# Kernel tuning notes

Measured on AMD Instinct MI355X. Metric: run time of the kernel, lower is better.

The kernel has to match this reference:

```python
import jax, jax.numpy as jnp
import numpy as np

QMIN, QMAX = 0.0, 255.0
# activation statistics (min, max) per layer, from init_kwargs['stats']
STATS = {"conv1": (-0.5, 3.0), "conv2": (0.0, 6.0), "fc1": (0.0, 8.0), "fc2": (0.0, 10.0)}


def calc_scale_zp(min_val, max_val):
    scale = (max_val - min_val) / (QMAX - QMIN)
    # original: int(clamped initial zero point) -> truncation
    zp = jnp.trunc(jnp.clip(QMIN - min_val / scale, QMIN, QMAX))
    return scale, zp


def quantize(x, min_val=None, max_val=None):
    if min_val is None:
        min_val, max_val = x.min(), x.max()
    scale, zp = calc_scale_zp(min_val, max_val)
    q = jnp.round(jnp.clip(zp + x / scale, QMIN, QMAX))
    return q, scale, zp


def conv2d(x, w, b):
    y = jax.lax.conv_general_dilated(x, w, (1, 1), "VALID",
                                     dimension_numbers=("NCHW", "OIHW", "NCHW"))
    return y + b[None, :, None, None]


def linear(x, w, b):
    return x @ w.T + b


def max_pool_2x2(x):
    return jax.lax.reduce_window(x, -jnp.inf, jax.lax.max, (1, 1, 2, 2), (1, 1, 2, 2), "VALID")


def quantize_layer(q_x, scale_x, zp_x, W, B, apply_fn, stat):
    # fake-quant weights/bias with their own min/max
    wq, scale_w, zp_w = quantize(W)
    bq, scale_b, zp_b = quantize(B)
    scale_next, zp_next = calc_scale_zp(stat[0], stat[1])
    X = q_x - zp_x
    W_eff = scale_x * scale_w * (wq - zp_w)
    B_eff = scale_b * (bq + zp_b)  # '+ zp_b' is faithful to the source
    y = jax.nn.relu(apply_fn(X, W_eff, B_eff) / scale_next + zp_next)
    # .round().byte() in torch wraps mod 256
    return jnp.mod(jnp.round(y), 256.0), scale_next, zp_next


def setup_inputs() -> dict:
    key = jax.random.key(0)
    ks = jax.random.split(key, 9)
    B = 4096
    return {
        "x": jax.random.normal(ks[0], (B, 1, 28, 28), jnp.float32),
        "conv1_w": jax.random.normal(ks[1], (20, 1, 5, 5), jnp.float32) * 0.1,
        "conv1_b": jax.random.normal(ks[2], (20,), jnp.float32) * 0.1,
        "conv2_w": jax.random.normal(ks[3], (50, 20, 5, 5), jnp.float32) * 0.05,
        "conv2_b": jax.random.normal(ks[4], (50,), jnp.float32) * 0.05,
        "fc1_w": jax.random.normal(ks[5], (500, 800), jnp.float32) * 0.03,
        "fc1_b": jax.random.normal(ks[6], (500,), jnp.float32) * 0.03,
        "fc2_w": jax.random.normal(ks[7], (10, 500), jnp.float32) * 0.05,
        "fc2_b": jax.random.normal(ks[8], (10,), jnp.float32) * 0.05,
    }


def reference(x, conv1_w, conv1_b, conv2_w, conv2_b, fc1_w, fc1_b, fc2_w, fc2_b):
    q, s, zp = quantize(x, STATS["conv1"][0], STATS["conv1"][1])
    q, s, zp = quantize_layer(q, s, zp, conv1_w, conv1_b, conv2d, STATS["conv2"])
    q = max_pool_2x2(q)                       # [B,20,12,12]
    q, s, zp = quantize_layer(q, s, zp, conv2_w, conv2_b, conv2d, STATS["fc1"])
    q = max_pool_2x2(q)                       # [B,50,4,4]
    q = q.reshape(-1, 4 * 4 * 50)             # [B,800]
    q, s, zp = quantize_layer(q, s, zp, fc1_w, fc1_b, linear, STATS["fc2"])
    xf = s * (q - zp)                         # dequantize
    logits = linear(xf, fc2_w, fc2_b)         # [B,10]
    return jax.nn.log_softmax(logits, axis=1)
```

## Files before the change

kernel.cpp:

```cpp
#include <hip/hip_runtime.h>
#include <cmath>

#define TPB 256
typedef float floatx4 __attribute__((ext_vector_type(4)));
typedef __bf16 bf16x8 __attribute__((ext_vector_type(8)));
typedef unsigned short ushort8 __attribute__((ext_vector_type(8)));
typedef unsigned short ushort_t;

#define OFF_PMN 16
#define OFF_PMX 96
#define OFF_B1 520
#define OFF_B2 544
#define OFF_B3 600
#define W1BF_BYTE 6144
#define W2BF_BYTE 8192
#define W3BF_BYTE 131072
#define Q2_BYTE  29360128ULL

#define S_X1 (3.5f/255.0f)
#define ZP_X1 36.0f
#define S_N1 (6.0f/255.0f)
#define S_N2 (8.0f/255.0f)
#define S_N3 (10.0f/255.0f)

#define XSTR 40

__device__ inline float qclip(float x, float s, float zp){
    return rintf(fminf(fmaxf(zp + x / s, 0.0f), 255.0f));
}
__device__ inline ushort_t bfbits(float v){
    return (ushort_t)(__float_as_uint(v) >> 16);
}

__global__ __launch_bounds__(TPB) void k_minmax(
        const float* c1w, const float* c1b, const float* c2w, const float* c2b,
        const float* f1w, const float* f1b, float* pmn, float* pmx){
    __shared__ float smn[TPB], smx[TPB];
    int bb = blockIdx.x, tid = threadIdx.x;
    const float* src; int n, sub, nsub;
    if      (bb == 0){ src=c1w; n=500;    sub=0;     nsub=1;  }
    else if (bb == 1){ src=c1b; n=20;     sub=0;     nsub=1;  }
    else if (bb <  6){ src=c2w; n=25000;  sub=bb-2;  nsub=4;  }
    else if (bb == 6){ src=c2b; n=50;     sub=0;     nsub=1;  }
    else if (bb < 71){ src=f1w; n=400000; sub=bb-7;  nsub=64; }
    else             { src=f1b; n=500;    sub=0;     nsub=1;  }
    float mn = INFINITY, mx = -INFINITY;
    for (int i = sub*TPB + tid; i < n; i += nsub*TPB){
        float v = src[i]; mn = fminf(mn, v); mx = fmaxf(mx, v);
    }
    smn[tid] = mn; smx[tid] = mx; __syncthreads();
    for (int s = TPB/2; s > 0; s >>= 1){
        if (tid < s){
            smn[tid] = fminf(smn[tid], smn[tid+s]);
            smx[tid] = fmaxf(smx[tid], smx[tid+s]);
        }
        __syncthreads();
    }
    if (tid == 0){ pmn[bb] = smn[0]; pmx[bb] = smx[0]; }
}

#define N_EFF 452157
__global__ __launch_bounds__(TPB) void k_make_eff(
        const float* c1w, const float* c1b, const float* c2w, const float* c2b,
        const float* f1w, const float* f1b, const float* pmn, const float* pmx,
        float* ws, ushort_t* w1bf, ushort_t* w2bf, ushort_t* w3bf){
    __shared__ float sS[6], sZ[6];
    int tid = threadIdx.x;
    int wv = tid >> 6, lane = tid & 63;
    const int starts[6] = {0,1,2,6,7,71};
    const int counts[6] = {1,1,4,1,64,1};
    #pragma unroll
    for (int rep = 0; rep < 2; ++rep){
        int t = wv + rep*4;
        if (t < 6){
            float mn = INFINITY, mx = -INFINITY;
            if (lane < counts[t]){ mn = pmn[starts[t]+lane]; mx = pmx[starts[t]+lane]; }
            #pragma unroll
            for (int off = 32; off > 0; off >>= 1){
                mn = fminf(mn, __shfl_xor(mn, off));
                mx = fmaxf(mx, __shfl_xor(mx, off));
            }
            if (lane == 0){
                float s = (mx - mn) / 255.0f;
                sS[t] = s;
                sZ[t] = truncf(fminf(fmaxf(0.0f - mn / s, 0.0f), 255.0f));
            }
        }
    }
    __syncthreads();

    int i = blockIdx.x * TPB + tid;
    if (i >= N_EFF) return;
    if (i < 1024){
        int n = i >> 5, k = i & 31;
        float v = 0.0f;
        if (n < 20 && k < 25) v = qclip(c1w[n*25 + k], sS[0], sZ[0]) - sZ[0];
        w1bf[i] = bfbits(v);
    } else if (i < 1044){
        int j = i - 1024;
        ws[OFF_B1 + j] = (sS[1] * (qclip(c1b[j], sS[1], sZ[1]) + sZ[1])) / S_N1;
    } else if (i < 42004){
        int j = i - 1044;
        int c = j >> 11, r = j & 2047, co = r >> 5, k = r & 31;
        int q = k >> 3, jj = k & 7;
        int tap, ci; bool valid;
        if (c < 13){ tap = 2*c + (q>>1); ci = (q&1)*8 + jj; valid = (tap < 25); }
        else       { tap = 4*(c-13) + q; ci = 16 + jj;      valid = (tap < 25) && (jj < 4); }
        valid = valid && (co < 50);
        float v = 0.0f;
        if (valid) v = qclip(c2w[(co*20 + ci)*25 + tap], sS[2], sZ[2]) - sZ[2];
        w2bf[j] = bfbits(v);
    } else if (i < 42054){
        int j = i - 42004;
        ws[OFF_B2 + j] = (sS[3] * (qclip(c2b[j], sS[3], sZ[3]) + sZ[3])) / S_N2;
    } else if (i < 451654){
        int j = i - 42054;
        int n = j / 800, k = j - 800*n;
        float v = 0.0f;
        if (n < 500) v = qclip(f1w[n*800 + k], sS[4], sZ[4]) - sZ[4];
        w3bf[j] = bfbits(v);
    } else if (i < 452154){
        int j = i - 451654;
        ws[OFF_B3 + j] = (sS[5] * (qclip(f1b[j], sS[5], sZ[5]) + sZ[5])) / S_N3;
    } else if (i == 452154){
        ws[0] = (S_N1 * sS[2]) / S_N2;
    } else if (i == 452155){
        ws[1] = (S_N2 * sS[4]) / S_N3;
    } else {
        ws[2] = (S_X1 * sS[0]) / S_N1;
    }
}

__global__ __launch_bounds__(TPB) void k_conv12(const float* x, const ushort_t* w1bf,
                                                const ushort_t* w2bt, const float* ws,
                                                ushort_t* q2bf, int B){
    __shared__ __align__(16) ushort_t xs[144*XSTR];
    __shared__ __align__(16) ushort_t xim[3136];
    int b = blockIdx.x, tid = threadIdx.x;
    int lane = tid & 63, wv = tid >> 6;
    int ln = lane & 15, quad = lane >> 4;

    for (int i = tid; i < 144; i += TPB){
        *(unsigned int*)(xs + i*XSTR + 20) = 0u;
        *(unsigned int*)(xs + i*XSTR + 22) = 0u;
    }

    const float* xb = x + (size_t)b * 784;
    for (int i = tid; i < 784; i += TPB){
        float v = xb[i];
        float q = rintf(fminf(fmaxf(ZP_X1 + v / S_X1, 0.0f), 255.0f));
        ushort_t bits = bfbits(q - ZP_X1);
        xim[i] = bits; xim[784 + i] = bits; xim[1568 + i] = bits; xim[2352 + i] = bits;
    }

    int offj[8]; bool vj[8];
    #pragma unroll
    for (int j = 0; j < 8; ++j){
        int k = quad*8 + j;
        vj[j] = (k < 25);
        int kh = k / 5, kw = k - 5*kh;
        offj[j] = vj[j] ? (kh*28 + kw) : 0;
    }
    const ushort_t* xq = xim + quad*784;

    ushort8 bw0 = *(const ushort8*)(w1bf + ln*32 + quad*8);
    ushort8 bw1 = *(const ushort8*)(w1bf + (16 + ln)*32 + quad*8);
    bf16x8 bf0 = __builtin_bit_cast(bf16x8, bw0);
    bf16x8 bf1 = __builtin_bit_cast(bf16x8, bw1);

    float K1 = ws[2];
    float B1_0 = ws[OFF_B1 + ln];
    float B1_1 = (ln < 4) ? ws[OFF_B1 + 16 + ln] : 0.0f;
    __syncthreads();

    for (int i = 0; i < 9; ++i){
        int mt = 9*wv + i;
        int m = mt*16 + ln;
        int p = m >> 2, crn = m & 3;
        int ph_ = p / 12, pw_ = p - 12*ph_;
        int oh = 2*ph_ + (crn >> 1), ow = 2*pw_ + (crn & 1);
        int base = oh*28 + ow;
        ushort8 aw;
        #pragma unroll
        for (int j = 0; j < 8; ++j)
            aw[j] = vj[j] ? xq[base + offj[j]] : (ushort_t)0;
        bf16x8 af = __builtin_bit_cast(bf16x8, aw);
        floatx4 z = (floatx4){0.f,0.f,0.f,0.f};
        floatx4 a0 = __builtin_amdgcn_mfma_f32_16x16x32_bf16(af, bf0, z, 0, 0, 0);
        floatx4 a1 = __builtin_amdgcn_mfma_f32_16x16x32_bf16(af, bf1, z, 0, 0, 0);

        int pp = mt*4 + quad;
        {
            unsigned int qv[4];
            #pragma unroll
            for (int r = 0; r < 4; ++r){
                float y = fmaxf(fmaf(a0[r], K1, B1_0), 0.0f);
                qv[r] = ((unsigned int)rintf(y)) & 255u;
            }
            unsigned int h0 = qv[0] > qv[1] ? qv[0] : qv[1];
            unsigned int h1 = qv[2] > qv[3] ? qv[2] : qv[3];
            unsigned int mx = h0 > h1 ? h0 : h1;
            xs[pp*XSTR + ln] = bfbits((float)mx);
        }
        if (ln < 4){
            unsigned int qv[4];
            #pragma unroll
            for (int r = 0; r < 4; ++r){
                float y = fmaxf(fmaf(a1[r], K1, B1_1), 0.0f);
                qv[r] = ((unsigned int)rintf(y)) & 255u;
            }
            unsigned int h0 = qv[0] > qv[1] ? qv[0] : qv[1];
            unsigned int h1 = qv[2] > qv[3] ? qv[2] : qv[3];
            unsigned int mx = h0 > h1 ? h0 : h1;
            xs[pp*XSTR + 16 + ln] = bfbits((float)mx);
        }
    }
    __syncthreads();

    int mt0 = (wv & 1) * 2;
    int nt0 = (wv >> 1) * 2;
    int abase[2];
    #pragma unroll
    for (int mi = 0; mi < 2; ++mi)
        abase[mi] = (24*(mt0+mi) + (ln>>3)*12 + (ln&7)) * XSTR;
    int aoff[20];
    #pragma unroll
    for (int c = 0; c < 20; ++c){
        int tap, inner;
        if (c < 13){ tap = 2*c + (quad>>1); inner = (quad&1)*8; }
        else       { tap = 4*(c-13) + quad; inner = 16; }
        int pt = 0;
        if (tap < 25){ int kh = tap/5, kw = tap-5*kh; pt = kh*12 + kw; }
        aoff[c] = pt*XSTR + inner;
    }

    float sc2d = ws[0];
    const ushort_t* bsrc0 = w2bt + (size_t)(nt0*16 + ln)*32 + quad*8;
    const ushort_t* bsrc1 = bsrc0 + 16*32;

    floatx4 acc[2][2];
    #pragma unroll
    for (int mi = 0; mi < 2; ++mi)
        #pragma unroll
        for (int ni = 0; ni < 2; ++ni) acc[mi][ni] = (floatx4){0.f,0.f,0.f,0.f};

    #pragma unroll
    for (int c = 0; c < 20; ++c){
        ushort8 b0w = *(const ushort8*)(bsrc0 + c*2048);
        ushort8 b1w = *(const ushort8*)(bsrc1 + c*2048);
        ushort8 a0w = *(const ushort8*)(xs + abase[0] + aoff[c]);
        ushort8 a1w = *(const ushort8*)(xs + abase[1] + aoff[c]);
        bf16x8 a0 = __builtin_bit_cast(bf16x8, a0w);
        bf16x8 a1 = __builtin_bit_cast(bf16x8, a1w);
        bf16x8 b0 = __builtin_bit_cast(bf16x8, b0w);
        bf16x8 b1 = __builtin_bit_cast(bf16x8, b1w);
        acc[0][0] = __builtin_amdgcn_mfma_f32_16x16x32_bf16(a0, b0, acc[0][0], 0, 0, 0);
        acc[0][1] = __builtin_amdgcn_mfma_f32_16x16x32_bf16(a0, b1, acc[0][1], 0, 0, 0);
        acc[1][0] = __builtin_amdgcn_mfma_f32_16x16x32_bf16(a1, b0, acc[1][0], 0, 0, 0);
        acc[1][1] = __builtin_amdgcn_mfma_f32_16x16x32_bf16(a1, b1, acc[1][1], 0, 0, 0);
    }

    #pragma unroll
    for (int ni = 0; ni < 2; ++ni){
        int co = (nt0 + ni)*16 + ln;
        float bias2d = (co < 50) ? ws[OFF_B2 + co] : 0.0f;
        #pragma unroll
        for (int mi = 0; mi < 2; ++mi){
            int mt = mt0 + mi;
            unsigned int qv[4];
            #pragma unroll
            for (int r = 0; r < 4; ++r){
                float y = fmaxf(fmaf(acc[mi][ni][r], sc2d, bias2d), 0.0f);
                qv[r] = ((unsigned int)rintf(y)) & 255u;
            }
            unsigned int h0 = qv[0] > qv[1] ? qv[0] : qv[1];
            unsigned int h1 = qv[2] > qv[3] ? qv[2] : qv[3];
            unsigned int p0 = (unsigned int)__shfl_xor((int)h0, 32);
            unsigned int p1 = (unsigned int)__shfl_xor((int)h1, 32);
            unsigned int v0 = h0 > p0 ? h0 : p0;
            unsigned int v1 = h1 > p1 ? h1 : p1;
            if (quad < 2 && co < 50){
                size_t base = (size_t)b*800 + co*16 + mt*4 + quad*2;
                q2bf[base]     = bfbits((float)v0);
                q2bf[base + 1] = bfbits((float)v1);
            }
        }
    }
}

__global__ __launch_bounds__(512) void k_fc12(const ushort_t* q2bf, const ushort_t* w3bf,
                                              const float* ws, const float* w2,
                                              const float* b2, float* out, int B){
    __shared__ float red[8*16*10];
    int tid = threadIdx.x;
    int lane = tid & 63, wv = tid >> 6;
    int ln = lane & 15, quad = lane >> 4;
    int b0 = blockIdx.x * 16;

    const ushort_t* asrc = q2bf + (size_t)(b0 + ln)*800 + quad*8;

    floatx4 acc[4];
    #pragma unroll
    for (int t = 0; t < 4; ++t) acc[t] = (floatx4){0.f,0.f,0.f,0.f};

    for (int c = 0; c < 25; ++c){
        ushort8 aw = *(const ushort8*)(asrc + c*32);
        bf16x8 af = __builtin_bit_cast(bf16x8, aw);
        #pragma unroll
        for (int t = 0; t < 4; ++t){
            int n = wv*64 + t*16 + ln;
            ushort8 bw = *(const ushort8*)(w3bf + (size_t)n*800 + c*32 + quad*8);
            acc[t] = __builtin_amdgcn_mfma_f32_16x16x32_bf16(
                         af, __builtin_bit_cast(bf16x8, bw), acc[t], 0, 0, 0);
        }
    }

    float sc3d = ws[1];
    float xf[4][4];
    #pragma unroll
    for (int t = 0; t < 4; ++t){
        int col = wv*64 + t*16 + ln;
        float bias = (col < 500) ? ws[OFF_B3 + col] : 0.0f;
        #pragma unroll
        for (int r = 0; r < 4; ++r){
            float y = fmaxf(fmaf(acc[t][r], sc3d, bias), 0.0f);
            unsigned int q = ((unsigned int)rintf(y)) & 255u;
            xf[r][t] = (col < 500) ? S_N3 * (float)q : 0.0f;
        }
    }

    #pragma unroll
    for (int c = 0; c < 10; ++c){
        float p[4] = {0.f, 0.f, 0.f, 0.f};
        #pragma unroll
        for (int t = 0; t < 4; ++t){
            int col = wv*64 + t*16 + ln;
            float w = (col < 500) ? w2[c*500 + col] : 0.0f;
            #pragma unroll
            for (int r = 0; r < 4; ++r) p[r] = fmaf(xf[r][t], w, p[r]);
        }
        #pragma unroll
        for (int m = 1; m <= 8; m <<= 1)
            #pragma unroll
            for (int r = 0; r < 4; ++r) p[r] += __shfl_xor(p[r], m);
        if (ln == 0){
            #pragma unroll
            for (int r = 0; r < 4; ++r)
                red[(wv*16 + quad*4 + r)*10 + c] = p[r];
        }
    }
    __syncthreads();

    if (tid < 16){
        int row = tid;
        float lg[10], mx = -INFINITY;
        #pragma unroll
        for (int c = 0; c < 10; ++c){
            float s = b2[c];
            #pragma unroll
            for (int w = 0; w < 8; ++w) s += red[(w*16 + row)*10 + c];
            lg[c] = s; mx = fmaxf(mx, s);
        }
        float sum = 0.0f;
        #pragma unroll
        for (int c = 0; c < 10; ++c) sum += expf(lg[c] - mx);
        float ls = logf(sum);
        #pragma unroll
        for (int c = 0; c < 10; ++c)
            out[(size_t)(b0 + row)*10 + c] = lg[c] - mx - ls;
    }
}

extern "C" void kernel_launch(void* const* d_in, const int* in_sizes, int n_in,
                              void* d_out, int out_size, void* d_ws, size_t ws_size,
                              hipStream_t stream){
    const float* x   = (const float*)d_in[0];
    const float* c1w = (const float*)d_in[1];
    const float* c1b = (const float*)d_in[2];
    const float* c2w = (const float*)d_in[3];
    const float* c2b = (const float*)d_in[4];
    const float* f1w = (const float*)d_in[5];
    const float* f1b = (const float*)d_in[6];
    const float* f2w = (const float*)d_in[7];
    const float* f2b = (const float*)d_in[8];
    int B = in_sizes[0] / 784;

    float* ws = (float*)d_ws;
    float* pmn = ws + OFF_PMN;
    float* pmx = ws + OFF_PMX;
    ushort_t* w1bf = (ushort_t*)((char*)d_ws + W1BF_BYTE);
    ushort_t* w2bf = (ushort_t*)((char*)d_ws + W2BF_BYTE);
    ushort_t* w3bf = (ushort_t*)((char*)d_ws + W3BF_BYTE);
    ushort_t* q2bf = (ushort_t*)((char*)d_ws + Q2_BYTE);
    float* out = (float*)d_out;

    k_minmax<<<72, TPB, 0, stream>>>(c1w, c1b, c2w, c2b, f1w, f1b, pmn, pmx);
    k_make_eff<<<(N_EFF + TPB - 1)/TPB, TPB, 0, stream>>>(c1w, c1b, c2w, c2b, f1w, f1b, pmn, pmx, ws, w1bf, w2bf, w3bf);
    k_conv12<<<B, TPB, 0, stream>>>(x, w1bf, w2bf, ws, q2bf, B);
    k_fc12<<<B/16, 512, 0, stream>>>(q2bf, w3bf, ws, f2w, f2b, out, B);
}
```

Measured before the change: 159.7 us.

## Split fc1 over column groups with partial logits; fast-path requant max-pool

The fc1 kernel now splits the 512 output columns into four groups handled by separate 256-thread blocks. Each block writes partial fc2 logits to a workspace buffer, and a new small kernel sums the partials and applies log-softmax. The conv epilogues max-pool in float before rounding, falling back to per-element wrap-around rounding only when a wave sees a value at or above 255.5. Conv1 im2col loads also drop the per-tap validity predicate and rely on zero-padded weights. The aim is more blocks for fc1 and fewer rounding operations, at the cost of an extra launch and partial-sum traffic.

Result: no change. 160.4 us (+0.5%).

```diff
diff --git a/kernel.cpp b/kernel.cpp
--- a/kernel.cpp
+++ b/kernel.cpp
@@ -15,6 +15,7 @@
 #define W1BF_BYTE 6144
 #define W2BF_BYTE 8192
 #define W3BF_BYTE 131072
+#define PART_BYTE 1048576
 #define Q2_BYTE  29360128ULL
 
 #define S_X1 (3.5f/255.0f)
@@ -24,6 +25,7 @@
 #define S_N3 (10.0f/255.0f)
 
 #define XSTR 40
+#define NCG 4
 
 __device__ inline float qclip(float x, float s, float zp){
     return rintf(fminf(fmaxf(zp + x / s, 0.0f), 255.0f));
@@ -153,13 +155,12 @@
         xim[i] = bits; xim[784 + i] = bits; xim[1568 + i] = bits; xim[2352 + i] = bits;
     }
 
-    int offj[8]; bool vj[8];
+    int offj[8];
     #pragma unroll
     for (int j = 0; j < 8; ++j){
         int k = quad*8 + j;
-        vj[j] = (k < 25);
         int kh = k / 5, kw = k - 5*kh;
-        offj[j] = vj[j] ? (kh*28 + kw) : 0;
+        offj[j] = (k < 25) ? (kh*28 + kw) : 0;
     }
     const ushort_t* xq = xim + quad*784;
 
@@ -183,7 +184,7 @@
         ushort8 aw;
         #pragma unroll
         for (int j = 0; j < 8; ++j)
-            aw[j] = vj[j] ? xq[base + offj[j]] : (ushort_t)0;
+            aw[j] = xq[base + offj[j]];
         bf16x8 af = __builtin_bit_cast(bf16x8, aw);
         floatx4 z = (floatx4){0.f,0.f,0.f,0.f};
         floatx4 a0 = __builtin_amdgcn_mfma_f32_16x16x32_bf16(af, bf0, z, 0, 0, 0);
@@ -191,28 +192,40 @@
 
         int pp = mt*4 + quad;
         {
-            unsigned int qv[4];
-            #pragma unroll
-            for (int r = 0; r < 4; ++r){
-                float y = fmaxf(fmaf(a0[r], K1, B1_0), 0.0f);
-                qv[r] = ((unsigned int)rintf(y)) & 255u;
-            }
-            unsigned int h0 = qv[0] > qv[1] ? qv[0] : qv[1];
-            unsigned int h1 = qv[2] > qv[3] ? qv[2] : qv[3];
-            unsigned int mx = h0 > h1 ? h0 : h1;
-            xs[pp*XSTR + ln] = bfbits((float)mx);
+            float y0 = fmaf(a0[0], K1, B1_0), y1 = fmaf(a0[1], K1, B1_0);
+            float y2 = fmaf(a0[2], K1, B1_0), y3 = fmaf(a0[3], K1, B1_0);
+            float mA = fmaxf(fmaxf(y0, y1), y2);
+            float mf = fmaxf(fmaxf(mA, y3), 0.0f);
+            if (__ballot(mf >= 255.5f)){
+                unsigned int q0 = ((unsigned int)rintf(fmaxf(y0,0.f))) & 255u;
+                unsigned int q1 = ((unsigned int)rintf(fmaxf(y1,0.f))) & 255u;
+                unsigned int qq2 = ((unsigned int)rintf(fmaxf(y2,0.f))) & 255u;
+                unsigned int q3 = ((unsigned int)rintf(fmaxf(y3,0.f))) & 255u;
+                unsigned int h0 = q0 > q1 ? q0 : q1;
+                unsigned int h1 = qq2 > q3 ? qq2 : q3;
+                mf = (float)(h0 > h1 ? h0 : h1);
+            } else {
+                mf = rintf(mf);
+            }
+            xs[pp*XSTR + ln] = bfbits(mf);
         }
         if (ln < 4){
-            unsigned int qv[4];
-            #pragma unroll
-            for (int r = 0; r < 4; ++r){
-                float y = fmaxf(fmaf(a1[r], K1, B1_1), 0.0f);
-                qv[r] = ((unsigned int)rintf(y)) & 255u;
-            }
-            unsigned int h0 = qv[0] > qv[1] ? qv[0] : qv[1];
-            unsigned int h1 = qv[2] > qv[3] ? qv[2] : qv[3];
-            unsigned int mx = h0 > h1 ? h0 : h1;
-            xs[pp*XSTR + 16 + ln] = bfbits((float)mx);
+            float y0 = fmaf(a1[0], K1, B1_1), y1 = fmaf(a1[1], K1, B1_1);
+            float y2 = fmaf(a1[2], K1, B1_1), y3 = fmaf(a1[3], K1, B1_1);
+            float mA = fmaxf(fmaxf(y0, y1), y2);
+            float mf = fmaxf(fmaxf(mA, y3), 0.0f);
+            if (__ballot(mf >= 255.5f)){
+                unsigned int q0 = ((unsigned int)rintf(fmaxf(y0,0.f))) & 255u;
+                unsigned int q1 = ((unsigned int)rintf(fmaxf(y1,0.f))) & 255u;
+                unsigned int qq2 = ((unsigned int)rintf(fmaxf(y2,0.f))) & 255u;
+                unsigned int q3 = ((unsigned int)rintf(fmaxf(y3,0.f))) & 255u;
+                unsigned int h0 = q0 > q1 ? q0 : q1;
+                unsigned int h1 = qq2 > q3 ? qq2 : q3;
+                mf = (float)(h0 > h1 ? h0 : h1);
+            } else {
+                mf = rintf(mf);
+            }
+            xs[pp*XSTR + 16 + ln] = bfbits(mf);
         }
     }
     __syncthreads();
@@ -267,59 +280,73 @@
         #pragma unroll
         for (int mi = 0; mi < 2; ++mi){
             int mt = mt0 + mi;
-            unsigned int qv[4];
-            #pragma unroll
-            for (int r = 0; r < 4; ++r){
-                float y = fmaxf(fmaf(acc[mi][ni][r], sc2d, bias2d), 0.0f);
-                qv[r] = ((unsigned int)rintf(y)) & 255u;
-            }
-            unsigned int h0 = qv[0] > qv[1] ? qv[0] : qv[1];
-            unsigned int h1 = qv[2] > qv[3] ? qv[2] : qv[3];
-            unsigned int p0 = (unsigned int)__shfl_xor((int)h0, 32);
-            unsigned int p1 = (unsigned int)__shfl_xor((int)h1, 32);
-            unsigned int v0 = h0 > p0 ? h0 : p0;
-            unsigned int v1 = h1 > p1 ? h1 : p1;
+            float y0 = fmaf(acc[mi][ni][0], sc2d, bias2d);
+            float y1 = fmaf(acc[mi][ni][1], sc2d, bias2d);
+            float y2 = fmaf(acc[mi][ni][2], sc2d, bias2d);
+            float y3 = fmaf(acc[mi][ni][3], sc2d, bias2d);
+            float f0 = fmaxf(fmaxf(y0, y1), 0.0f);
+            float f1 = fmaxf(fmaxf(y2, y3), 0.0f);
+            float g0 = __shfl_xor(f0, 32);
+            float g1 = __shfl_xor(f1, 32);
+            float v0f = fmaxf(f0, g0), v1f = fmaxf(f1, g1);
+            if (__ballot(fmaxf(v0f, v1f) >= 255.5f)){
+                unsigned int q0 = ((unsigned int)rintf(fmaxf(y0,0.f))) & 255u;
+                unsigned int q1 = ((unsigned int)rintf(fmaxf(y1,0.f))) & 255u;
+                unsigned int qq2 = ((unsigned int)rintf(fmaxf(y2,0.f))) & 255u;
+                unsigned int q3 = ((unsigned int)rintf(fmaxf(y3,0.f))) & 255u;
+                unsigned int h0 = q0 > q1 ? q0 : q1;
+                unsigned int h1 = qq2 > q3 ? qq2 : q3;
+                unsigned int p0 = (unsigned int)__shfl_xor((int)h0, 32);
+                unsigned int p1 = (unsigned int)__shfl_xor((int)h1, 32);
+                v0f = (float)(h0 > p0 ? h0 : p0);
+                v1f = (float)(h1 > p1 ? h1 : p1);
+            } else {
+                v0f = rintf(v0f); v1f = rintf(v1f);
+            }
             if (quad < 2 && co < 50){
                 size_t base = (size_t)b*800 + co*16 + mt*4 + quad*2;
-                q2bf[base]     = bfbits((float)v0);
-                q2bf[base + 1] = bfbits((float)v1);
-            }
-        }
-    }
-}
-
-__global__ __launch_bounds__(512) void k_fc12(const ushort_t* q2bf, const ushort_t* w3bf,
+                q2bf[base]     = bfbits(v0f);
+                q2bf[base + 1] = bfbits(v1f);
+            }
+        }
+    }
+}
+
+__global__ __launch_bounds__(256) void k_fc12(const ushort_t* q2bf, const ushort_t* w3bf,
                                               const float* ws, const float* w2,
-                                              const float* b2, float* out, int B){
-    __shared__ float red[8*16*10];
+                                              float* part, int B){
+    __shared__ float red[4*16*10];
     int tid = threadIdx.x;
     int lane = tid & 63, wv = tid >> 6;
     int ln = lane & 15, quad = lane >> 4;
-    int b0 = blockIdx.x * 16;
+    int bi = blockIdx.x;
+    int cg = bi & (NCG-1);
+    int b0 = (bi >> 2) * 16;
+    int n0 = cg*128 + wv*32;
 
     const ushort_t* asrc = q2bf + (size_t)(b0 + ln)*800 + quad*8;
-
-    floatx4 acc[4];
-    #pragma unroll
-    for (int t = 0; t < 4; ++t) acc[t] = (floatx4){0.f,0.f,0.f,0.f};
+    const ushort_t* bsrc = w3bf + (size_t)(n0 + ln)*800 + quad*8;
+
+    floatx4 acc[2];
+    acc[0] = (floatx4){0.f,0.f,0.f,0.f};
+    acc[1] = (floatx4){0.f,0.f,0.f,0.f};
 
     for (int c = 0; c < 25; ++c){
         ushort8 aw = *(const ushort8*)(asrc + c*32);
         bf16x8 af = __builtin_bit_cast(bf16x8, aw);
-        #pragma unroll
-        for (int t = 0; t < 4; ++t){
-            int n = wv*64 + t*16 + ln;
-            ushort8 bw = *(const ushort8*)(w3bf + (size_t)n*800 + c*32 + quad*8);
-            acc[t] = __builtin_amdgcn_mfma_f32_16x16x32_bf16(
-                         af, __builtin_bit_cast(bf16x8, bw), acc[t], 0, 0, 0);
-        }
+        ushort8 b0w = *(const ushort8*)(bsrc + c*32);
+        ushort8 b1w = *(const ushort8*)(bsrc + 16*800 + c*32);
+        acc[0] = __builtin_amdgcn_mfma_f32_16x16x32_bf16(
+                     af, __builtin_bit_cast(bf16x8, b0w), acc[0], 0, 0, 0);
+        acc[1] = __builtin_amdgcn_mfma_f32_16x16x32_bf16(
+                     af, __builtin_bit_cast(bf16x8, b1w), acc[1], 0, 0, 0);
     }
 
     float sc3d = ws[1];
-    float xf[4][4];
-    #pragma unroll
-    for (int t = 0; t < 4; ++t){
-        int col = wv*64 + t*16 + ln;
+    float xf[4][2];
+    #pragma unroll
+    for (int t = 0; t < 2; ++t){
+        int col = n0 + t*16 + ln;
         float bias = (col < 500) ? ws[OFF_B3 + col] : 0.0f;
         #pragma unroll
         for (int r = 0; r < 4; ++r){
@@ -333,8 +360,8 @@
     for (int c = 0; c < 10; ++c){
         float p[4] = {0.f, 0.f, 0.f, 0.f};
         #pragma unroll
-        for (int t = 0; t < 4; ++t){
-            int col = wv*64 + t*16 + ln;
+        for (int t = 0; t < 2; ++t){
+            int col = n0 + t*16 + ln;
             float w = (col < 500) ? w2[c*500 + col] : 0.0f;
             #pragma unroll
             for (int r = 0; r < 4; ++r) p[r] = fmaf(xf[r][t], w, p[r]);
@@ -351,24 +378,33 @@
     }
     __syncthreads();
 
-    if (tid < 16){
-        int row = tid;
-        float lg[10], mx = -INFINITY;
-        #pragma unroll
-        for (int c = 0; c < 10; ++c){
-            float s = b2[c];
-            #pragma unroll
-            for (int w = 0; w < 8; ++w) s += red[(w*16 + row)*10 + c];
-            lg[c] = s; mx = fmaxf(mx, s);
-        }
-        float sum = 0.0f;
-        #pragma unroll
-        for (int c = 0; c < 10; ++c) sum += expf(lg[c] - mx);
-        float ls = logf(sum);
-        #pragma unroll
-        for (int c = 0; c < 10; ++c)
-            out[(size_t)(b0 + row)*10 + c] = lg[c] - mx - ls;
-    }
+    if (tid < 160){
+        int row = tid / 10, c = tid - 10*(tid/10);
+        float s = red[row*10 + c] + red[160 + row*10 + c]
+                + red[320 + row*10 + c] + red[480 + row*10 + c];
+        part[((size_t)cg*B + b0 + row)*10 + c] = s;
+    }
+}
+
+__global__ __launch_bounds__(256) void k_softmax(const float* part, const float* b2,
+                                                 float* out, int B){
+    int i = blockIdx.x*256 + threadIdx.x;
+    if (i >= B) return;
+    float lg[10], mx = -INFINITY;
+    #pragma unroll
+    for (int c = 0; c < 10; ++c){
+        float s = b2[c];
+        #pragma unroll
+        for (int g = 0; g < NCG; ++g) s += part[((size_t)g*B + i)*10 + c];
+        lg[c] = s; mx = fmaxf(mx, s);
+    }
+    float sum = 0.0f;
+    #pragma unroll
+    for (int c = 0; c < 10; ++c) sum += expf(lg[c] - mx);
+    float ls = logf(sum);
+    #pragma unroll
+    for (int c = 0; c < 10; ++c)
+        out[(size_t)i*10 + c] = lg[c] - mx - ls;
 }
 
 extern "C" void kernel_launch(void* const* d_in, const int* in_sizes, int n_in,
@@ -391,11 +427,13 @@
     ushort_t* w1bf = (ushort_t*)((char*)d_ws + W1BF_BYTE);
     ushort_t* w2bf = (ushort_t*)((char*)d_ws + W2BF_BYTE);
     ushort_t* w3bf = (ushort_t*)((char*)d_ws + W3BF_BYTE);
+    float* part = (float*)((char*)d_ws + PART_BYTE);
     ushort_t* q2bf = (ushort_t*)((char*)d_ws + Q2_BYTE);
     float* out = (float*)d_out;
 
     k_minmax<<<72, TPB, 0, stream>>>(c1w, c1b, c2w, c2b, f1w, f1b, pmn, pmx);
     k_make_eff<<<(N_EFF + TPB - 1)/TPB, TPB, 0, stream>>>(c1w, c1b, c2w, c2b, f1w, f1b, pmn, pmx, ws, w1bf, w2bf, w3bf);
     k_conv12<<<B, TPB, 0, stream>>>(x, w1bf, w2bf, ws, q2bf, B);
-    k_fc12<<<B/16, 512, 0, stream>>>(q2bf, w3bf, ws, f2w, f2b, out, B);
-}
+    k_fc12<<<(B/16)*NCG, 256, 0, stream>>>(q2bf, w3bf, ws, f2w, part, B);
+    k_softmax<<<(B + 255)/256, 256, 0, stream>>>(part, f2b, out, B);
+}
```
